# Performance work log

Measured on AMD Instinct MI355X. Metric: run time of the kernel, lower is better.

The kernel has to match this reference:

```python
import jax, jax.numpy as jnp
import numpy as np

DIM = 1024
HEADS = 16
HEAD_DIM = DIM // HEADS
D_FF = 4 * DIM
EPS = 1e-5


def _layernorm(x, g, b):
    mu = jnp.mean(x, axis=-1, keepdims=True)
    var = jnp.mean(jnp.square(x - mu), axis=-1, keepdims=True)
    return (x - mu) * jax.lax.rsqrt(var + EPS) * g + b


def setup_inputs() -> dict:
    key = jax.random.key(0)
    ks = jax.random.split(key, 8)
    s = 0.02
    return {
        "x": jax.random.normal(ks[0], (2, 2048, DIM), dtype=jnp.float32),
        "Wqkv": jax.random.normal(ks[1], (DIM, 3 * DIM), dtype=jnp.float32) * s,
        "bqkv": jnp.zeros((3 * DIM,), dtype=jnp.float32),
        "Wout": jax.random.normal(ks[2], (DIM, DIM), dtype=jnp.float32) * s,
        "bout": jnp.zeros((DIM,), dtype=jnp.float32),
        "W1": jax.random.normal(ks[3], (DIM, D_FF), dtype=jnp.float32) * s,
        "b1": jnp.zeros((D_FF,), dtype=jnp.float32),
        "W2": jax.random.normal(ks[4], (D_FF, DIM), dtype=jnp.float32) * s,
        "b2": jnp.zeros((DIM,), dtype=jnp.float32),
        "g1": jnp.ones((DIM,), dtype=jnp.float32),
        "be1": jnp.zeros((DIM,), dtype=jnp.float32),
        "g2": jnp.ones((DIM,), dtype=jnp.float32),
        "be2": jnp.zeros((DIM,), dtype=jnp.float32),
    }


def reference(x, Wqkv, bqkv, Wout, bout, W1, b1, W2, b2, g1, be1, g2, be2):
    B, T, C = x.shape
    # --- multi-head self-attention (explicit QK^T softmax, no mask/cache) ---
    qkv = (x @ Wqkv + bqkv).reshape(B, T, 3, HEADS, HEAD_DIM)
    q = qkv[:, :, 0].transpose(0, 2, 1, 3)  # (B,H,T,hd)
    k = qkv[:, :, 1].transpose(0, 2, 1, 3)
    v = qkv[:, :, 2].transpose(0, 2, 1, 3)
    scale = HEAD_DIM ** -0.5
    scores = jnp.einsum("bhqd,bhkd->bhqk", q, k) * scale  # (B,H,T,T)
    attn = jax.nn.softmax(scores, axis=-1)
    o = jnp.einsum("bhqk,bhkd->bhqd", attn, v)
    o = o.transpose(0, 2, 1, 3).reshape(B, T, C)
    attn_out = o @ Wout + bout
    # --- Post-LN: LN applied to sublayer output, then residual ---
    x = x + _layernorm(attn_out, g1, be1)
    # --- FFN with exact GELU ---
    h = jax.nn.gelu(x @ W1 + b1, approximate=False)
    ffn_out = h @ W2 + b2
    x = x + _layernorm(ffn_out, g2, be2)
    return x
```

## Files before the change

### kernel.cpp

```cpp
#include <hip/hip_runtime.h>
#include <cstdint>
#include <cstddef>

#define DIM 1024
#define HEADS 16
#define HD 64
#define DFF 4096
#define TSEQ 2048
#define EPS 1e-5f

#define WAITCNT_VM4 0xF74
#define WAITCNT_VM0 0xF70
#define WAITCNT_VM8 0xF78
#define WAITCNT_LGKM0 0xC07F

typedef __bf16 bf16x8 __attribute__((ext_vector_type(8)));
typedef float floatx4 __attribute__((ext_vector_type(4)));

__device__ __forceinline__ unsigned short f2bf(float f) {
  union { float f; unsigned int u; } v; v.f = f;
  return (unsigned short)((v.u + 0x7FFFu + ((v.u >> 16) & 1u)) >> 16);
}

__device__ __forceinline__ float exp2_fast(float x) {
#if __has_builtin(__builtin_amdgcn_exp2f)
  return __builtin_amdgcn_exp2f(x);
#else
  float r;
  asm("v_exp_f32 %0, %1" : "=v"(r) : "v"(x));
  return r;
#endif
}

__device__ __forceinline__ float gelu_f(float v) {
  const float u = v * (0.7978845608f + 0.0356774081f * v * v);
  const float e = __expf(2.0f * u);
  const float t = 1.0f - 2.0f / (e + 1.0f);
  return 0.5f * v * (1.0f + t);
}

__device__ __forceinline__ void async16(const void* g, void* l) {
  __builtin_amdgcn_global_load_lds(
      (const __attribute__((address_space(1))) void*)g,
      (__attribute__((address_space(3))) void*)l, 16, 0, 0);
}

__global__ __launch_bounds__(256) void prep_all(const float* __restrict__ x,
                                                const float* __restrict__ Wqkv,
                                                const float* __restrict__ Wout,
                                                const float* __restrict__ W1,
                                                const float* __restrict__ W2,
                                                unsigned short* __restrict__ xb,
                                                unsigned short* __restrict__ WqkvT,
                                                unsigned short* __restrict__ WoutT,
                                                unsigned short* __restrict__ W1T,
                                                unsigned short* __restrict__ W2T) {
  const int bid = blockIdx.x;
  const int tid = threadIdx.x;
  if (bid < 4096) {
    const int i = bid * 256 + tid;
    float4 v = ((const float4*)x)[i];
    ushort4 o;
    o.x = f2bf(v.x); o.y = f2bf(v.y); o.z = f2bf(v.z); o.w = f2bf(v.w);
    ((ushort4*)xb)[i] = o;
    return;
  }
  int id = bid - 4096;
  const float* src; unsigned short* dst; int R, C, gx;
  if (id < 3072)      {            src = Wqkv; dst = WqkvT; R = 1024; C = 3072; gx = 96; }
  else if (id < 4096) { id -= 3072; src = Wout; dst = WoutT; R = 1024; C = 1024; gx = 32; }
  else if (id < 8192) { id -= 4096; src = W1;   dst = W1T;   R = 1024; C = 4096; gx = 128; }
  else                { id -= 8192; src = W2;   dst = W2T;   R = 4096; C = 1024; gx = 32; }
  const int c0 = (id % gx) * 32, r0 = (id / gx) * 32;
  const int tx = tid & 31, ty = tid >> 5;
  __shared__ float tile[32][33];
#pragma unroll
  for (int i = 0; i < 32; i += 8)
    tile[ty + i][tx] = src[(size_t)(r0 + ty + i) * C + c0 + tx];
  __syncthreads();
#pragma unroll
  for (int i = 0; i < 32; i += 8)
    dst[(size_t)(c0 + ty + i) * R + r0 + tx] = f2bf(tile[tx][ty + i]);
}

#define PIPELINED_KLOOP(NIT)                                                         \
  auto issue = [&](int s, int k0) {                                                  \
    async16(Ab0 + k0, &lds[s][tid * 8]);                                             \
    async16(Ab1 + k0, &lds[s][2048 + tid * 8]);                                      \
    async16(Bb0 + k0, &lds[s][4096 + tid * 8]);                                      \
    async16(Bb1 + k0, &lds[s][6144 + tid * 8]);                                      \
  };                                                                                 \
  issue(0, 0);                                                                       \
  int sidx = 0;                                                                      \
  for (int k = 0; k < (NIT); k++) {                                                  \
    if (k + 1 < (NIT)) {                                                             \
      issue(sidx ^ 1, (k + 1) * 32);                                                 \
      __builtin_amdgcn_s_waitcnt(WAITCNT_VM4);                                       \
    } else {                                                                         \
      __builtin_amdgcn_s_waitcnt(WAITCNT_VM0);                                       \
    }                                                                                \
    __builtin_amdgcn_s_barrier();                                                    \
    bf16x8 af[4], bg[4];                                                             \
    _Pragma("unroll")                                                                \
    for (int mi = 0; mi < 4; mi++)                                                   \
      af[mi] = *(const bf16x8*)&lds[sidx][(wm + mi * 16 + l16) * 32 + quad * 8];     \
    _Pragma("unroll")                                                                \
    for (int ni = 0; ni < 4; ni++)                                                   \
      bg[ni] = *(const bf16x8*)&lds[sidx][4096 + (wn + ni * 16 + l16) * 32 + quad * 8]; \
    _Pragma("unroll")                                                                \
    for (int mi = 0; mi < 4; mi++)                                                   \
      _Pragma("unroll")                                                              \
      for (int ni = 0; ni < 4; ni++)                                                 \
        acc[mi][ni] =                                                                \
            __builtin_amdgcn_mfma_f32_16x16x32_bf16(af[mi], bg[ni], acc[mi][ni], 0, 0, 0); \
    __builtin_amdgcn_s_waitcnt(WAITCNT_LGKM0);                                       \
    __builtin_amdgcn_s_barrier();                                                    \
    sidx ^= 1;                                                                       \
  }

template <int EPI>
__global__ __launch_bounds__(256) void gemm_bt(const unsigned short* __restrict__ A,
                                               const unsigned short* __restrict__ Bt,
                                               const float* __restrict__ bias,
                                               void* __restrict__ Cout,
                                               int M, int N, int K) {
  __shared__ unsigned short lds[2][8192];
  const int tid = threadIdx.x;
  const int bm = blockIdx.y * 128, bn = blockIdx.x * 128;
  const int wave = tid >> 6, lane = tid & 63;
  const int l16 = lane & 15, quad = lane >> 4;
  const int wm = (wave >> 1) * 64, wn = (wave & 1) * 64;

  floatx4 acc[4][4] = {};

  const int srow = tid >> 2;
  const int scol = (tid & 3) * 8;

  const unsigned short* Ab0 = A + (size_t)(bm + srow) * K + scol;
  const unsigned short* Ab1 = A + (size_t)(bm + 64 + srow) * K + scol;
  const unsigned short* Bb0 = Bt + (size_t)(bn + srow) * K + scol;
  const unsigned short* Bb1 = Bt + (size_t)(bn + 64 + srow) * K + scol;

  const int nit = K >> 5;
  PIPELINED_KLOOP(nit)
  __syncthreads();

  if (EPI == 0) {
#pragma unroll
    for (int ni = 0; ni < 4; ni++) {
      const int col = bn + wn + ni * 16 + l16;
      const float bv = bias[col];
#pragma unroll
      for (int mi = 0; mi < 4; mi++) {
        const int row0 = bm + wm + mi * 16 + quad * 4;
#pragma unroll
        for (int r = 0; r < 4; r++)
          ((float*)Cout)[(size_t)(row0 + r) * N + col] = acc[mi][ni][r] + bv;
      }
    }
  } else {
    unsigned short* eb = &lds[0][wave * 1152];
    float bvv[4];
#pragma unroll
    for (int ni = 0; ni < 4; ni++) bvv[ni] = bias[bn + wn + ni * 16 + l16];
    const int lrow = lane >> 2, ck = lane & 3;
#pragma unroll
    for (int mi = 0; mi < 4; mi++) {
#pragma unroll
      for (int ni = 0; ni < 4; ni++)
#pragma unroll
        for (int r = 0; r < 4; r++)
          eb[(quad * 4 + r) * 72 + ni * 16 + l16] =
              f2bf(gelu_f(acc[mi][ni][r] + bvv[ni]));
      __syncthreads();
      unsigned short* gp =
          (unsigned short*)Cout + (size_t)(bm + wm + mi * 16 + lrow) * N + bn + wn;
#pragma unroll
      for (int j = 0; j < 2; j++)
        *(uint4*)(gp + j * 32 + ck * 8) = *(const uint4*)&eb[lrow * 72 + j * 32 + ck * 8];
      __syncthreads();
    }
  }
}

__global__ __launch_bounds__(256) void gemm_splitk(const unsigned short* __restrict__ A,
                                                   const unsigned short* __restrict__ Bt,
                                                   float* __restrict__ Cp,
                                                   int M, int N, int Ktot, int Ksl) {
  __shared__ unsigned short lds[2][8192];
  const int tid = threadIdx.x;
  const int bm = blockIdx.y * 128, bn = blockIdx.x * 128;
  const int koff = blockIdx.z * Ksl;
  const int wave = tid >> 6, lane = tid & 63;
  const int l16 = lane & 15, quad = lane >> 4;
  const int wm = (wave >> 1) * 64, wn = (wave & 1) * 64;

  floatx4 acc[4][4] = {};

  const int srow = tid >> 2;
  const int scol = (tid & 3) * 8;

  const unsigned short* Ab0 = A + (size_t)(bm + srow) * Ktot + koff + scol;
  const unsigned short* Ab1 = A + (size_t)(bm + 64 + srow) * Ktot + koff + scol;
  const unsigned short* Bb0 = Bt + (size_t)(bn + srow) * Ktot + koff + scol;
  const unsigned short* Bb1 = Bt + (size_t)(bn + 64 + srow) * Ktot + koff + scol;

  const int nit = Ksl >> 5;
  PIPELINED_KLOOP(nit)

  float* out = Cp + (size_t)blockIdx.z * M * (size_t)N;
#pragma unroll
  for (int ni = 0; ni < 4; ni++) {
    const int col = bn + wn + ni * 16 + l16;
#pragma unroll
    for (int mi = 0; mi < 4; mi++) {
      const int row0 = bm + wm + mi * 16 + quad * 4;
#pragma unroll
      for (int r = 0; r < 4; r++)
        out[(size_t)(row0 + r) * N + col] = acc[mi][ni][r];
    }
  }
}

__global__ __launch_bounds__(256) void gemm_qkv(const unsigned short* __restrict__ A,
                                                const unsigned short* __restrict__ Bt,
                                                const float* __restrict__ bias,
                                                unsigned short* __restrict__ Qg,
                                                unsigned short* __restrict__ Kg,
                                                unsigned short* __restrict__ Vtg) {
  const int K = 1024;
  __shared__ unsigned short lds[2][8192];
  const int tid = threadIdx.x;
  const int bm = blockIdx.y * 128, bn = blockIdx.x * 128;
  const int wave = tid >> 6, lane = tid & 63;
  const int l16 = lane & 15, quad = lane >> 4;
  const int wm = (wave >> 1) * 64, wn = (wave & 1) * 64;

  floatx4 acc[4][4] = {};

  const int srow = tid >> 2;
  const int scol = (tid & 3) * 8;

  const unsigned short* Ab0 = A + (size_t)(bm + srow) * K + scol;
  const unsigned short* Ab1 = A + (size_t)(bm + 64 + srow) * K + scol;
  const unsigned short* Bb0 = Bt + (size_t)(bn + srow) * K + scol;
  const unsigned short* Bb1 = Bt + (size_t)(bn + 64 + srow) * K + scol;

  const int nit = K >> 5;
  PIPELINED_KLOOP(nit)

  const float QSCALE = 0.125f * 1.44269504089f;
#pragma unroll
  for (int ni = 0; ni < 4; ni++) {
    const int col = bn + wn + ni * 16 + l16;
    const float bv = bias[col];
    const int sec = col >> 10;
    const int cc = col & 1023;
    const int hh = cc >> 6, dd = cc & 63;
#pragma unroll
    for (int mi = 0; mi < 4; mi++) {
      const int row0 = bm + wm + mi * 16 + quad * 4;
      const int b2 = row0 >> 11, tt0 = row0 & 2047;
      if (sec == 0) {
        unsigned short* q = Qg + ((size_t)(b2 * HEADS + hh) * TSEQ + tt0) * HD + dd;
#pragma unroll
        for (int r = 0; r < 4; r++)
          q[(size_t)r * HD] = f2bf((acc[mi][ni][r] + bv) * QSCALE);
      } else if (sec == 1) {
        unsigned short* k = Kg + ((size_t)(b2 * HEADS + hh) * TSEQ + tt0) * HD + dd;
#pragma unroll
        for (int r = 0; r < 4; r++)
          k[(size_t)r * HD] = f2bf(acc[mi][ni][r] + bv);
      } else {
        ushort4 o;
        o.x = f2bf(acc[mi][ni][0] + bv);
        o.y = f2bf(acc[mi][ni][1] + bv);
        o.z = f2bf(acc[mi][ni][2] + bv);
        o.w = f2bf(acc[mi][ni][3] + bv);
        *(ushort4*)(Vtg + ((size_t)(b2 * HEADS + hh) * HD + dd) * TSEQ + tt0) = o;
      }
    }
  }
}

__global__ __launch_bounds__(256, 4) void attn_mfma(const unsigned short* __restrict__ Qg,
                                                    const unsigned short* __restrict__ Kg,
                                                    const unsigned short* __restrict__ Vtg,
                                                    unsigned short* __restrict__ ob) {
  __shared__ __align__(16) char smem[40960];
  unsigned short* QPs = (unsigned short*)smem;

  const int bid = blockIdx.x;
  const int lid = (bid & 7) * 128 + (bid >> 3);
  const int qt = lid & 31;
  const int h = (lid >> 5) & 15;
  const int b = lid >> 9;
  const int tid = threadIdx.x;
  const int w = tid >> 6, lane = tid & 63, l16 = lane & 15, quad = lane >> 4;
  const int qg = w >> 1;
  const int kh = w & 1;

  const int r0 = tid >> 3;
  const int c0 = (tid & 7) ^ (r0 & 7);

  const char* Qbase = (const char*)(Qg + ((size_t)(b * HEADS + h) * TSEQ + qt * 64) * HD);
  const char* Kbase = (const char*)(Kg + (size_t)(b * HEADS + h) * TSEQ * HD);
  const char* Vbase = (const char*)(Vtg + (size_t)(b * HEADS + h) * HD * TSEQ);

  auto Ksp = [&](int s) -> char* { return smem + 8192 + s * 8192; };
  auto Vsp = [&](int s) -> char* { return smem + 24576 + s * 8192; };

  auto issueKV = [&](int s, int ch) {
    const size_t koff = (size_t)ch * 64;
#pragma unroll
    for (int i = 0; i < 2; i++) {
      async16(Kbase + (koff + r0 + i * 32) * 128 + c0 * 16, Ksp(s) + (i * 256 + tid) * 16);
      async16(Vbase + (size_t)(r0 + i * 32) * (TSEQ * 2) + koff * 2 + c0 * 16,
              Vsp(s) + (i * 256 + tid) * 16);
    }
  };

#pragma unroll
  for (int i = 0; i < 2; i++)
    async16(Qbase + (size_t)(r0 + i * 32) * 128 + c0 * 16, (char*)QPs + (i * 256 + tid) * 16);
  issueKV(0, 0);
  issueKV(1, 1);

  __builtin_amdgcn_s_waitcnt(WAITCNT_VM8);
  __builtin_amdgcn_s_barrier();

  bf16x8 qf[2][2];
#pragma unroll
  for (int mi = 0; mi < 2; mi++)
#pragma unroll
    for (int kt = 0; kt < 2; kt++) {
      const int row = qg * 32 + mi * 16 + l16;
      qf[mi][kt] = *(const bf16x8*)((const char*)QPs + row * 128 +
                                    (((quad + 4 * kt) ^ (row & 7)) * 16));
    }
  __builtin_amdgcn_s_waitcnt(WAITCNT_LGKM0);
  __builtin_amdgcn_sched_barrier(0);

  union { unsigned short u[8]; bf16x8 b; } onesu;
#pragma unroll
  for (int j = 0; j < 8; j++) onesu.u[j] = 0x3F80;
  const bf16x8 ones = onesu.b;

  floatx4 oacc[2][5] = {};
  char* Pw = (char*)QPs + w * 2048;

  const int NC = TSEQ / 64;
  int sidx = 0;
  for (int ch = 0; ch < NC; ch++) {
    if (ch < NC - 1) __builtin_amdgcn_s_waitcnt(WAITCNT_VM4);
    else             __builtin_amdgcn_s_waitcnt(WAITCNT_VM0);
    __builtin_amdgcn_s_barrier();

    floatx4 sacc[2][2] = {};
    __builtin_amdgcn_s_setprio(1);
#pragma unroll
    for (int kt = 0; kt < 2; kt++) {
#pragma unroll
      for (int ni = 0; ni < 2; ni++) {
        const int krow = kh * 32 + ni * 16 + l16;
        bf16x8 kf = *(const bf16x8*)(Ksp(sidx) + krow * 128 +
                                     (((quad + 4 * kt) ^ (krow & 7)) * 16));
#pragma unroll
        for (int mi = 0; mi < 2; mi++)
          sacc[mi][ni] =
              __builtin_amdgcn_mfma_f32_16x16x32_bf16(qf[mi][kt], kf, sacc[mi][ni], 0, 0, 0);
      }
    }
    __builtin_amdgcn_s_setprio(0);

#pragma unroll
    for (int mi = 0; mi < 2; mi++)
#pragma unroll
      for (int ni = 0; ni < 2; ni++)
#pragma unroll
        for (int r = 0; r < 4; r++) {
          const float p = exp2_fast(sacc[mi][ni][r]);
          const unsigned int pu = __builtin_bit_cast(unsigned int, p);
          const int row = mi * 16 + quad * 4 + r;
          *((unsigned short*)(Pw + row * 64 +
                              (((ni * 2 + (l16 >> 3)) ^ quad) * 16) + (l16 & 7) * 2)) =
              (unsigned short)(pu >> 16);
        }

    __builtin_amdgcn_s_setprio(1);
    bf16x8 pf[2];
#pragma unroll
    for (int mi = 0; mi < 2; mi++) {
      const int prow = mi * 16 + l16;
      pf[mi] = *(const bf16x8*)(Pw + prow * 64 + ((quad ^ ((l16 >> 2) & 3)) * 16));
    }
#pragma unroll
    for (int nj = 0; nj < 4; nj++) {
      const int vrow = nj * 16 + l16;
      bf16x8 vf = *(const bf16x8*)(Vsp(sidx) + vrow * 128 +
                                   (((quad + 4 * kh) ^ (vrow & 7)) * 16));
#pragma unroll
      for (int mi = 0; mi < 2; mi++)
        oacc[mi][nj] = __builtin_amdgcn_mfma_f32_16x16x32_bf16(pf[mi], vf, oacc[mi][nj], 0, 0, 0);
    }
#pragma unroll
    for (int mi = 0; mi < 2; mi++)
      oacc[mi][4] = __builtin_amdgcn_mfma_f32_16x16x32_bf16(pf[mi], ones, oacc[mi][4], 0, 0, 0);
    __builtin_amdgcn_s_setprio(0);

    __builtin_amdgcn_s_waitcnt(WAITCNT_LGKM0);
    __builtin_amdgcn_s_barrier();
    if (ch + 2 < NC) issueKV(sidx, ch + 2);
    sidx ^= 1;
  }

  __syncthreads();
  float* Op = (float*)smem + qg * (32 * 66);
  if (kh == 1) {
#pragma unroll
    for (int mi = 0; mi < 2; mi++)
#pragma unroll
      for (int r = 0; r < 4; r++) {
        const int row = mi * 16 + quad * 4 + r;
#pragma unroll
        for (int nj = 0; nj < 4; nj++)
          Op[row * 66 + nj * 16 + l16] = oacc[mi][nj][r];
        if (l16 == 0) Op[row * 66 + 64] = oacc[mi][4][r];
      }
  }
  __syncthreads();
  if (kh == 0) {
#pragma unroll
    for (int mi = 0; mi < 2; mi++)
#pragma unroll
      for (int r = 0; r < 4; r++) {
        const int row = mi * 16 + quad * 4 + r;
        const float inv = 1.0f / (oacc[mi][4][r] + Op[row * 66 + 64]);
        const int t = qt * 64 + qg * 32 + row;
        unsigned short* orow = ob + (size_t)(b * TSEQ + t) * DIM + h * HD + l16;
#pragma unroll
        for (int nj = 0; nj < 4; nj++)
          orow[nj * 16] = f2bf((oacc[mi][nj][r] + Op[row * 66 + nj * 16 + l16]) * inv);
      }
  }
}

template <int NP, int WBF>
__global__ __launch_bounds__(256) void add_ln_red(const float* __restrict__ xin,
                                                  const float* __restrict__ parts,
                                                  const float* __restrict__ bias,
                                                  const float* __restrict__ gw,
                                                  const float* __restrict__ bw,
                                                  float* __restrict__ xout,
                                                  unsigned short* __restrict__ xbf) {
  const size_t MN = (size_t)4096 * DIM;
  const int row = blockIdx.x;
  const int tid = threadIdx.x;
  const int c = tid * 4;
  const size_t base = (size_t)row * DIM;
  float4 v = *(const float4*)(parts + base + c);
#pragma unroll
  for (int p = 1; p < NP; p++) {
    float4 t = *(const float4*)(parts + p * MN + base + c);
    v.x += t.x; v.y += t.y; v.z += t.z; v.w += t.w;
  }
  float4 bb = *(const float4*)(bias + c);
  v.x += bb.x; v.y += bb.y; v.z += bb.z; v.w += bb.w;

  float s = v.x + v.y + v.z + v.w;
  float s2 = v.x * v.x + v.y * v.y + v.z * v.z + v.w * v.w;
#pragma unroll
  for (int off = 1; off < 64; off <<= 1) {
    s += __shfl_xor(s, off);
    s2 += __shfl_xor(s2, off);
  }
  __shared__ float rsum[4], rsq[4];
  if ((tid & 63) == 0) { rsum[tid >> 6] = s; rsq[tid >> 6] = s2; }
  __syncthreads();
  s = rsum[0] + rsum[1] + rsum[2] + rsum[3];
  s2 = rsq[0] + rsq[1] + rsq[2] + rsq[3];
  const float mu = s * (1.0f / DIM);
  const float var = s2 * (1.0f / DIM) - mu * mu;
  const float rstd = rsqrtf(var + EPS);
  float4 xv = *(const float4*)(xin + base + c);
  float4 gv = *(const float4*)(gw + c);
  float4 bv = *(const float4*)(bw + c);
  float4 o;
  o.x = xv.x + (v.x - mu) * rstd * gv.x + bv.x;
  o.y = xv.y + (v.y - mu) * rstd * gv.y + bv.y;
  o.z = xv.z + (v.z - mu) * rstd * gv.z + bv.z;
  o.w = xv.w + (v.w - mu) * rstd * gv.w + bv.w;
  *(float4*)(xout + base + c) = o;
  if (WBF) {
    ushort4 ob;
    ob.x = f2bf(o.x); ob.y = f2bf(o.y); ob.z = f2bf(o.z); ob.w = f2bf(o.w);
    *(ushort4*)(xbf + base + c) = ob;
  }
}

extern "C" void kernel_launch(void* const* d_in, const int* in_sizes, int n_in,
                              void* d_out, int out_size, void* d_ws, size_t ws_size,
                              hipStream_t stream) {
  const float* x    = (const float*)d_in[0];
  const float* Wqkv = (const float*)d_in[1];
  const float* bqkv = (const float*)d_in[2];
  const float* Wout = (const float*)d_in[3];
  const float* bout = (const float*)d_in[4];
  const float* W1   = (const float*)d_in[5];
  const float* b1   = (const float*)d_in[6];
  const float* W2   = (const float*)d_in[7];
  const float* b2   = (const float*)d_in[8];
  const float* g1   = (const float*)d_in[9];
  const float* be1  = (const float*)d_in[10];
  const float* g2   = (const float*)d_in[11];
  const float* be2  = (const float*)d_in[12];

  char* w = (char*)d_ws;
  const size_t MB = 1048576;
  unsigned short* xb     = (unsigned short*)(w + 0 * MB);
  unsigned short* WqkvT  = (unsigned short*)(w + 8 * MB);
  unsigned short* WoutT  = (unsigned short*)(w + 14 * MB);
  unsigned short* W1T    = (unsigned short*)(w + 16 * MB);
  unsigned short* W2T    = (unsigned short*)(w + 24 * MB);
  unsigned short* Qb     = (unsigned short*)(w + 32 * MB);
  unsigned short* Kb     = (unsigned short*)(w + 40 * MB);
  unsigned short* Vtb    = (unsigned short*)(w + 48 * MB);
  unsigned short* obuf   = (unsigned short*)(w + 64 * MB);
  float*          atno_p = (float*)(w + 72 * MB);
  float*          x1     = (float*)(w + 0 * MB);
  unsigned short* x1b    = (unsigned short*)(w + 32 * MB);
  unsigned short* hb     = (unsigned short*)(w + 40 * MB);
  float*          ffn_p  = (float*)(w + 72 * MB);

  prep_all<<<16384, 256, 0, stream>>>(x, Wqkv, Wout, W1, W2, xb, WqkvT, WoutT, W1T, W2T);

  gemm_qkv<<<dim3(24, 32), 256, 0, stream>>>(xb, WqkvT, bqkv, Qb, Kb, Vtb);
  attn_mfma<<<1024, 256, 0, stream>>>(Qb, Kb, Vtb, obuf);
  gemm_splitk<<<dim3(8, 32, 4), 256, 0, stream>>>(obuf, WoutT, atno_p, 4096, 1024, 1024, 256);
  add_ln_red<4, 1><<<4096, 256, 0, stream>>>(x, atno_p, bout, g1, be1, x1, x1b);
  gemm_bt<1><<<dim3(32, 32), 256, 0, stream>>>(x1b, W1T, b1, hb, 4096, 4096, 1024);
  gemm_splitk<<<dim3(8, 32, 4), 256, 0, stream>>>(hb, W2T, ffn_p, 4096, 1024, 4096, 1024);
  add_ln_red<4, 0><<<4096, 256, 0, stream>>>(x1, ffn_p, b2, g2, be2, (float*)d_out, nullptr);
}
```

Baseline: 384.1 us.

## Replace 128x128 GEMMs with 256x256 tile 512-thread swizzled-LDS GEMM core

All four GEMMs move from a 128x128 tile with 256 threads and 32-wide K steps to a shared 256x256 tile core with 512 threads, 64-wide K steps, XOR-swizzled LDS and 128KB of dynamic shared memory, double-buffered. Block indices are remapped so neighbouring tiles land on the same XCD for L2 reuse. The aim is higher arithmetic intensity per byte loaded and fewer LDS bank conflicts. The trade-off is a large LDS footprint that limits occupancy, plus fewer blocks (256 for the 4096x4096 GEMM) for the tail. The attention P staging also switches to a padded layout read back with two 8-byte loads, and the workspace layout is reshuffled.

```diff
diff --git a/kernel.cpp b/kernel.cpp
--- a/kernel.cpp
+++ b/kernel.cpp
@@ -15,6 +15,7 @@
 #define WAITCNT_LGKM0 0xC07F
 
 typedef __bf16 bf16x8 __attribute__((ext_vector_type(8)));
+typedef __bf16 bf16x4 __attribute__((ext_vector_type(4)));
 typedef float floatx4 __attribute__((ext_vector_type(4)));
 
 __device__ __forceinline__ unsigned short f2bf(float f) {
@@ -83,183 +84,142 @@
     dst[(size_t)(c0 + ty + i) * R + r0 + tx] = f2bf(tile[tx][ty + i]);
 }
 
-#define PIPELINED_KLOOP(NIT)                                                         \
-  auto issue = [&](int s, int k0) {                                                  \
-    async16(Ab0 + k0, &lds[s][tid * 8]);                                             \
-    async16(Ab1 + k0, &lds[s][2048 + tid * 8]);                                      \
-    async16(Bb0 + k0, &lds[s][4096 + tid * 8]);                                      \
-    async16(Bb1 + k0, &lds[s][6144 + tid * 8]);                                      \
-  };                                                                                 \
-  issue(0, 0);                                                                       \
-  int sidx = 0;                                                                      \
-  for (int k = 0; k < (NIT); k++) {                                                  \
-    if (k + 1 < (NIT)) {                                                             \
-      issue(sidx ^ 1, (k + 1) * 32);                                                 \
-      __builtin_amdgcn_s_waitcnt(WAITCNT_VM4);                                       \
-    } else {                                                                         \
-      __builtin_amdgcn_s_waitcnt(WAITCNT_VM0);                                       \
-    }                                                                                \
-    __builtin_amdgcn_s_barrier();                                                    \
-    bf16x8 af[4], bg[4];                                                             \
-    _Pragma("unroll")                                                                \
-    for (int mi = 0; mi < 4; mi++)                                                   \
-      af[mi] = *(const bf16x8*)&lds[sidx][(wm + mi * 16 + l16) * 32 + quad * 8];     \
-    _Pragma("unroll")                                                                \
-    for (int ni = 0; ni < 4; ni++)                                                   \
-      bg[ni] = *(const bf16x8*)&lds[sidx][4096 + (wn + ni * 16 + l16) * 32 + quad * 8]; \
-    _Pragma("unroll")                                                                \
-    for (int mi = 0; mi < 4; mi++)                                                   \
-      _Pragma("unroll")                                                              \
-      for (int ni = 0; ni < 4; ni++)                                                 \
-        acc[mi][ni] =                                                                \
-            __builtin_amdgcn_mfma_f32_16x16x32_bf16(af[mi], bg[ni], acc[mi][ni], 0, 0, 0); \
-    __builtin_amdgcn_s_waitcnt(WAITCNT_LGKM0);                                       \
-    __builtin_amdgcn_s_barrier();                                                    \
-    sidx ^= 1;                                                                       \
-  }
-
-template <int EPI>
-__global__ __launch_bounds__(256) void gemm_bt(const unsigned short* __restrict__ A,
-                                               const unsigned short* __restrict__ Bt,
-                                               const float* __restrict__ bias,
-                                               void* __restrict__ Cout,
-                                               int M, int N, int K) {
-  __shared__ unsigned short lds[2][8192];
+#define GEMM256_CORE(APTR, BPTR, KT, KOFF, NG_)                                       \
+  const int lane = tid & 63, wv = tid >> 6;                                           \
+  const int l16 = lane & 15, quad = lane >> 4;                                        \
+  const int wr = wv >> 2, wc = wv & 3;                                                \
+  const int srow = tid >> 3;                                                          \
+  const int scc = (tid & 7) ^ (srow & 7);                                             \
+  const unsigned short* Asrc = (APTR) + (size_t)(bm + srow) * (KT) + (KOFF) + scc * 8;\
+  const unsigned short* Bsrc = (BPTR) + (size_t)(bn + srow) * (KT) + (KOFF) + scc * 8;\
+  auto stageKstep = [&](int buf, int kk) {                                            \
+    char* dA = smem + buf * 65536;                                                    \
+    char* dB = dA + 32768;                                                            \
+    _Pragma("unroll")                                                                 \
+    for (int h = 0; h < 2; h++)                                                       \
+      _Pragma("unroll")                                                               \
+      for (int j = 0; j < 2; j++) {                                                   \
+        async16(Asrc + (size_t)(h * 128 + 64 * j) * (KT) + kk,                        \
+                dA + h * 16384 + (j * 512 + tid) * 16);                               \
+        async16(Bsrc + (size_t)(h * 128 + 64 * j) * (KT) + kk,                        \
+                dB + h * 16384 + (j * 512 + tid) * 16);                               \
+      }                                                                               \
+  };                                                                                  \
+  floatx4 acc[8][4] = {};                                                             \
+  stageKstep(0, 0);                                                                   \
+  __builtin_amdgcn_s_waitcnt(WAITCNT_VM0);                                            \
+  __builtin_amdgcn_s_barrier();                                                       \
+  for (int g = 0; g < (NG_); g++) {                                                   \
+    const int p = g & 1;                                                              \
+    const char* Ab = smem + p * 65536 + wr * 16384;                                   \
+    const char* Bb = smem + p * 65536 + 32768 + (wc >> 1) * 16384;                    \
+    bf16x8 bg[4][2];                                                                  \
+    _Pragma("unroll")                                                                 \
+    for (int q = 0; q < 4; q++) {                                                     \
+      if (q == 0) {                                                                   \
+        if (g + 1 < (NG_)) stageKstep(p ^ 1, (g + 1) << 6);                           \
+        _Pragma("unroll")                                                             \
+        for (int ni = 0; ni < 4; ni++) {                                              \
+          const int lr = (wc & 1) * 64 + ni * 16 + l16;                               \
+          _Pragma("unroll")                                                           \
+          for (int ks = 0; ks < 2; ks++)                                              \
+            bg[ni][ks] = *(const bf16x8*)(Bb + lr * 128 +                             \
+                                          (((quad + 4 * ks) ^ (lr & 7)) * 16));       \
+        }                                                                             \
+      }                                                                               \
+      bf16x8 af[2][2];                                                                \
+      _Pragma("unroll")                                                               \
+      for (int m = 0; m < 2; m++) {                                                   \
+        const int lr = (q * 2 + m) * 16 + l16;                                        \
+        _Pragma("unroll")                                                             \
+        for (int ks = 0; ks < 2; ks++)                                                \
+          af[m][ks] = *(const bf16x8*)(Ab + lr * 128 +                                \
+                                       (((quad + 4 * ks) ^ (lr & 7)) * 16));          \
+      }                                                                               \
+      __builtin_amdgcn_s_barrier();                                                   \
+      __builtin_amdgcn_s_waitcnt(WAITCNT_LGKM0);                                      \
+      __builtin_amdgcn_s_setprio(1);                                                  \
+      _Pragma("unroll")                                                               \
+      for (int ks = 0; ks < 2; ks++)                                                  \
+        _Pragma("unroll")                                                             \
+        for (int ni = 0; ni < 4; ni++)                                                \
+          _Pragma("unroll")                                                           \
+          for (int m = 0; m < 2; m++)                                                 \
+            acc[q * 2 + m][ni] = __builtin_amdgcn_mfma_f32_16x16x32_bf16(             \
+                af[m][ks], bg[ni][ks], acc[q * 2 + m][ni], 0, 0, 0);                  \
+      __builtin_amdgcn_s_setprio(0);                                                  \
+      if (q == 3) __builtin_amdgcn_s_waitcnt(WAITCNT_VM0);                            \
+      __builtin_amdgcn_s_barrier();                                                   \
+    }                                                                                 \
+  }
+
+__global__ __launch_bounds__(512, 2) void gemm256g(const unsigned short* __restrict__ A,
+                                                   const unsigned short* __restrict__ Bt,
+                                                   const float* __restrict__ bias,
+                                                   unsigned short* __restrict__ Cout,
+                                                   int M, int N, int K) {
+  extern __shared__ char smem[];
   const int tid = threadIdx.x;
-  const int bm = blockIdx.y * 128, bn = blockIdx.x * 128;
-  const int wave = tid >> 6, lane = tid & 63;
-  const int l16 = lane & 15, quad = lane >> 4;
-  const int wm = (wave >> 1) * 64, wn = (wave & 1) * 64;
-
-  floatx4 acc[4][4] = {};
-
-  const int srow = tid >> 2;
-  const int scol = (tid & 3) * 8;
-
-  const unsigned short* Ab0 = A + (size_t)(bm + srow) * K + scol;
-  const unsigned short* Ab1 = A + (size_t)(bm + 64 + srow) * K + scol;
-  const unsigned short* Bb0 = Bt + (size_t)(bn + srow) * K + scol;
-  const unsigned short* Bb1 = Bt + (size_t)(bn + 64 + srow) * K + scol;
-
-  const int nit = K >> 5;
-  PIPELINED_KLOOP(nit)
+  int bxx = blockIdx.x, byy = blockIdx.y;
+  {
+    const int id = byy * 16 + bxx;
+    const int xcd = id & 7, sub = id >> 3;
+    bxx = (xcd & 3) * 4 + (sub & 3);
+    byy = (xcd >> 2) * 8 + (sub >> 2);
+  }
+  const int bm = byy * 256, bn = bxx * 256;
+  GEMM256_CORE(A, Bt, K, 0, K >> 6)
+
   __syncthreads();
-
-  if (EPI == 0) {
-#pragma unroll
-    for (int ni = 0; ni < 4; ni++) {
-      const int col = bn + wn + ni * 16 + l16;
-      const float bv = bias[col];
-#pragma unroll
-      for (int mi = 0; mi < 4; mi++) {
-        const int row0 = bm + wm + mi * 16 + quad * 4;
-#pragma unroll
-        for (int r = 0; r < 4; r++)
-          ((float*)Cout)[(size_t)(row0 + r) * N + col] = acc[mi][ni][r] + bv;
-      }
-    }
-  } else {
-    unsigned short* eb = &lds[0][wave * 1152];
-    float bvv[4];
-#pragma unroll
-    for (int ni = 0; ni < 4; ni++) bvv[ni] = bias[bn + wn + ni * 16 + l16];
-    const int lrow = lane >> 2, ck = lane & 3;
-#pragma unroll
-    for (int mi = 0; mi < 4; mi++) {
-#pragma unroll
-      for (int ni = 0; ni < 4; ni++)
-#pragma unroll
-        for (int r = 0; r < 4; r++)
-          eb[(quad * 4 + r) * 72 + ni * 16 + l16] =
-              f2bf(gelu_f(acc[mi][ni][r] + bvv[ni]));
-      __syncthreads();
-      unsigned short* gp =
-          (unsigned short*)Cout + (size_t)(bm + wm + mi * 16 + lrow) * N + bn + wn;
-#pragma unroll
-      for (int j = 0; j < 2; j++)
-        *(uint4*)(gp + j * 32 + ck * 8) = *(const uint4*)&eb[lrow * 72 + j * 32 + ck * 8];
-      __syncthreads();
-    }
-  }
-}
-
-__global__ __launch_bounds__(256) void gemm_splitk(const unsigned short* __restrict__ A,
-                                                   const unsigned short* __restrict__ Bt,
-                                                   float* __restrict__ Cp,
-                                                   int M, int N, int Ktot, int Ksl) {
-  __shared__ unsigned short lds[2][8192];
+  unsigned short* eb = (unsigned short*)smem + wv * 1152;
+  float bvv[4];
+#pragma unroll
+  for (int ni = 0; ni < 4; ni++) bvv[ni] = bias[bn + wc * 64 + ni * 16 + l16];
+  const int lrow = lane >> 2, ck = lane & 3;
+#pragma unroll
+  for (int mi = 0; mi < 8; mi++) {
+#pragma unroll
+    for (int ni = 0; ni < 4; ni++)
+#pragma unroll
+      for (int r = 0; r < 4; r++)
+        eb[(quad * 4 + r) * 72 + ni * 16 + l16] =
+            f2bf(gelu_f(acc[mi][ni][r] + bvv[ni]));
+    __syncthreads();
+    unsigned short* gp =
+        Cout + (size_t)(bm + wr * 128 + mi * 16 + lrow) * N + bn + wc * 64;
+#pragma unroll
+    for (int j = 0; j < 2; j++)
+      *(uint4*)(gp + j * 32 + ck * 8) = *(const uint4*)&eb[lrow * 72 + j * 32 + ck * 8];
+    __syncthreads();
+  }
+}
+
+__global__ __launch_bounds__(512, 2) void gemm256_qkv(const unsigned short* __restrict__ A,
+                                                      const unsigned short* __restrict__ Bt,
+                                                      const float* __restrict__ bias,
+                                                      unsigned short* __restrict__ Qg,
+                                                      unsigned short* __restrict__ Kg,
+                                                      unsigned short* __restrict__ Vtg) {
+  extern __shared__ char smem[];
   const int tid = threadIdx.x;
-  const int bm = blockIdx.y * 128, bn = blockIdx.x * 128;
-  const int koff = blockIdx.z * Ksl;
-  const int wave = tid >> 6, lane = tid & 63;
-  const int l16 = lane & 15, quad = lane >> 4;
-  const int wm = (wave >> 1) * 64, wn = (wave & 1) * 64;
-
-  floatx4 acc[4][4] = {};
-
-  const int srow = tid >> 2;
-  const int scol = (tid & 3) * 8;
-
-  const unsigned short* Ab0 = A + (size_t)(bm + srow) * Ktot + koff + scol;
-  const unsigned short* Ab1 = A + (size_t)(bm + 64 + srow) * Ktot + koff + scol;
-  const unsigned short* Bb0 = Bt + (size_t)(bn + srow) * Ktot + koff + scol;
-  const unsigned short* Bb1 = Bt + (size_t)(bn + 64 + srow) * Ktot + koff + scol;
-
-  const int nit = Ksl >> 5;
-  PIPELINED_KLOOP(nit)
-
-  float* out = Cp + (size_t)blockIdx.z * M * (size_t)N;
+  const int id = blockIdx.y * 12 + blockIdx.x;
+  const int xcd = id / 24, sub = id % 24;
+  const int bxx = (xcd & 3) * 3 + sub % 3;
+  const int byy = (xcd >> 2) * 8 + sub / 3;
+  const int bm = byy * 256, bn = bxx * 256;
+  GEMM256_CORE(A, Bt, 1024, 0, 16)
+
+  const float QSCALE = 0.125f * 1.44269504089f;
 #pragma unroll
   for (int ni = 0; ni < 4; ni++) {
-    const int col = bn + wn + ni * 16 + l16;
-#pragma unroll
-    for (int mi = 0; mi < 4; mi++) {
-      const int row0 = bm + wm + mi * 16 + quad * 4;
-#pragma unroll
-      for (int r = 0; r < 4; r++)
-        out[(size_t)(row0 + r) * N + col] = acc[mi][ni][r];
-    }
-  }
-}
-
-__global__ __launch_bounds__(256) void gemm_qkv(const unsigned short* __restrict__ A,
-                                                const unsigned short* __restrict__ Bt,
-                                                const float* __restrict__ bias,
-                                                unsigned short* __restrict__ Qg,
-                                                unsigned short* __restrict__ Kg,
-                                                unsigned short* __restrict__ Vtg) {
-  const int K = 1024;
-  __shared__ unsigned short lds[2][8192];
-  const int tid = threadIdx.x;
-  const int bm = blockIdx.y * 128, bn = blockIdx.x * 128;
-  const int wave = tid >> 6, lane = tid & 63;
-  const int l16 = lane & 15, quad = lane >> 4;
-  const int wm = (wave >> 1) * 64, wn = (wave & 1) * 64;
-
-  floatx4 acc[4][4] = {};
-
-  const int srow = tid >> 2;
-  const int scol = (tid & 3) * 8;
-
-  const unsigned short* Ab0 = A + (size_t)(bm + srow) * K + scol;
-  const unsigned short* Ab1 = A + (size_t)(bm + 64 + srow) * K + scol;
-  const unsigned short* Bb0 = Bt + (size_t)(bn + srow) * K + scol;
-  const unsigned short* Bb1 = Bt + (size_t)(bn + 64 + srow) * K + scol;
-
-  const int nit = K >> 5;
-  PIPELINED_KLOOP(nit)
-
-  const float QSCALE = 0.125f * 1.44269504089f;
-#pragma unroll
-  for (int ni = 0; ni < 4; ni++) {
-    const int col = bn + wn + ni * 16 + l16;
+    const int col = bn + wc * 64 + ni * 16 + l16;
     const float bv = bias[col];
     const int sec = col >> 10;
     const int cc = col & 1023;
     const int hh = cc >> 6, dd = cc & 63;
 #pragma unroll
-    for (int mi = 0; mi < 4; mi++) {
-      const int row0 = bm + wm + mi * 16 + quad * 4;
+    for (int mi = 0; mi < 8; mi++) {
+      const int row0 = bm + wr * 128 + mi * 16 + quad * 4;
       const int b2 = row0 >> 11, tt0 = row0 & 2047;
       if (sec == 0) {
         unsigned short* q = Qg + ((size_t)(b2 * HEADS + hh) * TSEQ + tt0) * HD + dd;
@@ -283,6 +243,35 @@
   }
 }
 
+__global__ __launch_bounds__(512, 2) void gemm256_sk(const unsigned short* __restrict__ A,
+                                                     const unsigned short* __restrict__ Bt,
+                                                     float* __restrict__ Cp,
+                                                     int M, int N, int Ktot, int Ksl) {
+  extern __shared__ char smem[];
+  const int tid = threadIdx.x;
+  const int id = (blockIdx.z * 16 + blockIdx.y) * 4 + blockIdx.x;
+  const int xcd = id >> 5, sub = id & 31;
+  const int bxx = sub & 3;
+  const int u = xcd * 8 + (sub >> 2);
+  const int byy = u & 15, bz = u >> 4;
+  const int bm = byy * 256, bn = bxx * 256;
+  const int koff = bz * Ksl;
+  GEMM256_CORE(A, Bt, Ktot, koff, Ksl >> 6)
+
+  float* out = Cp + (size_t)bz * M * (size_t)N;
+#pragma unroll
+  for (int ni = 0; ni < 4; ni++) {
+    const int col = bn + wc * 64 + ni * 16 + l16;
+#pragma unroll
+    for (int mi = 0; mi < 8; mi++) {
+      const int row0 = bm + wr * 128 + mi * 16 + quad * 4;
+#pragma unroll
+      for (int r = 0; r < 4; r++)
+        out[(size_t)(row0 + r) * N + col] = acc[mi][ni][r];
+    }
+  }
+}
+
 __global__ __launch_bounds__(256, 4) void attn_mfma(const unsigned short* __restrict__ Qg,
                                                     const unsigned short* __restrict__ Kg,
                                                     const unsigned short* __restrict__ Vtg,
@@ -347,7 +336,7 @@
   const bf16x8 ones = onesu.b;
 
   floatx4 oacc[2][5] = {};
-  char* Pw = (char*)QPs + w * 2048;
+  char* Pw = (char*)QPs + w * 1152;
 
   const int NC = TSEQ / 64;
   int sidx = 0;
@@ -373,27 +362,25 @@
     }
     __builtin_amdgcn_s_setprio(0);
 
-#pragma unroll
-    for (int mi = 0; mi < 2; mi++)
+    bf16x8 pf[2];
+#pragma unroll
+    for (int mi = 0; mi < 2; mi++) {
 #pragma unroll
       for (int ni = 0; ni < 2; ni++)
 #pragma unroll
         for (int r = 0; r < 4; r++) {
           const float p = exp2_fast(sacc[mi][ni][r]);
           const unsigned int pu = __builtin_bit_cast(unsigned int, p);
-          const int row = mi * 16 + quad * 4 + r;
-          *((unsigned short*)(Pw + row * 64 +
-                              (((ni * 2 + (l16 >> 3)) ^ quad) * 16) + (l16 & 7) * 2)) =
+          *((unsigned short*)(Pw + (quad * 4 + r) * 72 + (ni * 16 + l16) * 2)) =
               (unsigned short)(pu >> 16);
         }
+      union { bf16x8 v8; bf16x4 v4[2]; } u;
+      u.v4[0] = *(const bf16x4*)(Pw + l16 * 72 + quad * 16);
+      u.v4[1] = *(const bf16x4*)(Pw + l16 * 72 + quad * 16 + 8);
+      pf[mi] = u.v8;
+    }
 
     __builtin_amdgcn_s_setprio(1);
-    bf16x8 pf[2];
-#pragma unroll
-    for (int mi = 0; mi < 2; mi++) {
-      const int prow = mi * 16 + l16;
-      pf[mi] = *(const bf16x8*)(Pw + prow * 64 + ((quad ^ ((l16 >> 2) & 3)) * 16));
-    }
 #pragma unroll
     for (int nj = 0; nj < 4; nj++) {
       const int vrow = nj * 16 + l16;
@@ -515,6 +502,17 @@
   const float* g2   = (const float*)d_in[11];
   const float* be2  = (const float*)d_in[12];
 
+  static bool s_attr = false;
+  if (!s_attr) {
+    hipFuncSetAttribute((const void*)gemm256g,
+                        hipFuncAttributeMaxDynamicSharedMemorySize, 131072);
+    hipFuncSetAttribute((const void*)gemm256_qkv,
+                        hipFuncAttributeMaxDynamicSharedMemorySize, 131072);
+    hipFuncSetAttribute((const void*)gemm256_sk,
+                        hipFuncAttributeMaxDynamicSharedMemorySize, 131072);
+    s_attr = true;
+  }
+
   char* w = (char*)d_ws;
   const size_t MB = 1048576;
   unsigned short* xb     = (unsigned short*)(w + 0 * MB);
@@ -527,18 +525,18 @@
   unsigned short* Vtb    = (unsigned short*)(w + 48 * MB);
   unsigned short* obuf   = (unsigned short*)(w + 64 * MB);
   float*          atno_p = (float*)(w + 72 * MB);
-  float*          x1     = (float*)(w + 0 * MB);
-  unsigned short* x1b    = (unsigned short*)(w + 32 * MB);
-  unsigned short* hb     = (unsigned short*)(w + 40 * MB);
+  float*          x1     = (float*)(w + 136 * MB);
+  unsigned short* x1b    = (unsigned short*)(w + 152 * MB);
+  unsigned short* hb     = (unsigned short*)(w + 32 * MB);
   float*          ffn_p  = (float*)(w + 72 * MB);
 
   prep_all<<<16384, 256, 0, stream>>>(x, Wqkv, Wout, W1, W2, xb, WqkvT, WoutT, W1T, W2T);
 
-  gemm_qkv<<<dim3(24, 32), 256, 0, stream>>>(xb, WqkvT, bqkv, Qb, Kb, Vtb);
+  gemm256_qkv<<<dim3(12, 16), 512, 131072, stream>>>(xb, WqkvT, bqkv, Qb, Kb, Vtb);
   attn_mfma<<<1024, 256, 0, stream>>>(Qb, Kb, Vtb, obuf);
-  gemm_splitk<<<dim3(8, 32, 4), 256, 0, stream>>>(obuf, WoutT, atno_p, 4096, 1024, 1024, 256);
+  gemm256_sk<<<dim3(4, 16, 4), 512, 131072, stream>>>(obuf, WoutT, atno_p, 4096, 1024, 1024, 256);
   add_ln_red<4, 1><<<4096, 256, 0, stream>>>(x, atno_p, bout, g1, be1, x1, x1b);
-  gemm_bt<1><<<dim3(32, 32), 256, 0, stream>>>(x1b, W1T, b1, hb, 4096, 4096, 1024);
-  gemm_splitk<<<dim3(8, 32, 4), 256, 0, stream>>>(hb, W2T, ffn_p, 4096, 1024, 4096, 1024);
+  gemm256g<<<dim3(16, 16), 512, 131072, stream>>>(x1b, W1T, b1, hb, 4096, 4096, 1024);
+  gemm256_sk<<<dim3(4, 16, 4), 512, 131072, stream>>>(hb, W2T, ffn_p, 4096, 1024, 4096, 1024);
   add_ln_red<4, 0><<<4096, 256, 0, stream>>>(x1, ffn_p, b2, g2, be2, (float*)d_out, nullptr);
 }
```

Measured after the change: 362.7 us. 5.6% less time.
